# Kernel tuning notes

Measured on AMD Instinct MI355X. Metric: run time of the kernel, lower is better.

## Reference

```python
import jax, jax.numpy as jnp
import numpy as np

B, S = 64, 4096
IN_CH, HID, OUT_CH, LIFT, MODES, NLAYERS = 2, 64, 3, 256, 16, 4
FREQ = S // 2 + 1


def setup_inputs() -> dict:
    key = jax.random.key(0)
    ks = jax.random.split(key, 10)
    g = lambda k, shp, s=0.02: (jax.random.normal(k, shp, jnp.float32) * s)
    return {
        "x": jax.random.normal(ks[0], (B, S, IN_CH), jnp.float32),
        "lift_w1": g(ks[1], (LIFT, IN_CH), 0.1),
        "lift_b1": jnp.zeros((LIFT,), jnp.float32),
        "lift_w2": g(ks[2], (HID, LIFT)),
        "lift_b2": jnp.zeros((HID,), jnp.float32),
        # spectral weights per layer: real/imag parts of [in, out, modes]
        "spec_wr": g(ks[3], (NLAYERS, HID, HID, MODES), 1.0 / HID),
        "spec_wi": g(ks[4], (NLAYERS, HID, HID, MODES), 1.0 / HID),
        "skip_w": g(ks[5], (NLAYERS, HID, HID)),
        "skip_b": jnp.zeros((NLAYERS, HID), jnp.float32),
        "proj_w1": g(ks[6], (LIFT, HID)),
        "proj_b1": jnp.zeros((LIFT,), jnp.float32),
        "proj_w2": g(ks[7], (OUT_CH, LIFT)),
        "proj_b2": jnp.zeros((OUT_CH,), jnp.float32),
    }


def _gelu(x):
    return jax.nn.gelu(x, approximate=False)  # torch F.gelu default (exact)


def reference(x, lift_w1, lift_b1, lift_w2, lift_b2, spec_wr, spec_wi,
              skip_w, skip_b, proj_w1, proj_b1, proj_w2, proj_b2):
    # x: (B, S, 2) -> permute to channels-first (B, 2, S), fused into einsum
    h = jnp.einsum('bsi,oi->bos', x, lift_w1) + lift_b1[None, :, None]  # (B, 256, S)
    h = _gelu(h)
    h = jnp.einsum('bcs,oc->bos', h, lift_w2) + lift_b2[None, :, None]  # (B, 64, S)

    for l in range(NLAYERS):
        # spectral conv: rfft -> keep low modes -> complex mix -> irfft
        xf = jnp.fft.rfft(h, axis=-1)[..., :MODES]            # (B, HID, MODES) complex
        w = spec_wr[l] + 1j * spec_wi[l]                       # (HID, HID, MODES)
        yk = jnp.einsum('bim,iom->bom', xf, w)                 # (B, HID, MODES)
        yf = jnp.zeros((h.shape[0], HID, FREQ), jnp.complex64).at[..., :MODES].set(yk)
        spec = jnp.fft.irfft(yf, n=S, axis=-1)                 # (B, HID, S)
        skip = jnp.einsum('bcs,oc->bos', h, skip_w[l]) + skip_b[l][None, :, None]
        h = spec + skip
        if l < NLAYERS - 1:
            h = _gelu(h)

    h = _gelu(jnp.einsum('bcs,oc->bos', h, proj_w1) + proj_b1[None, :, None])
    out_seq = jnp.einsum('bcs,oc->bos', h, proj_w2) + proj_b2[None, :, None]  # (B, 3, S)
    # AdaptiveAvgPool1d(1) + squeeze(-1) == mean over length
    return out_seq.mean(axis=-1)  # (B, 3)
```

## Files before the change

### kernel.cpp

```cpp
#include <hip/hip_runtime.h>
#include <math.h>

#define B_    64
#define S_    4096
#define HID   64
#define LIFT  256
#define MODES 16
#define NL    4

#define OFF_H     0
#define OFF_ETB   16777216
#define OFF_XFY   (OFF_ETB + 131072)
#define OFF_SKH   (OFF_XFY + 131072)
#define OFF_SKL   (OFF_SKH + 8192)
#define OFF_W2HI  (OFF_SKL + 8192)
#define OFF_W2LO  (OFF_W2HI + 8192)
#define OFF_P1HI  (OFF_W2LO + 8192)
#define OFF_P1LO  (OFF_P1HI + 8192)
#define OFF_PART  (OFF_P1LO + 8192)
#define OFF_W1B   (OFF_PART + 12288)

typedef short short8 __attribute__((ext_vector_type(8)));
typedef float f32x4  __attribute__((ext_vector_type(4)));
typedef unsigned uint8v __attribute__((ext_vector_type(8)));
#define MFMA16 __builtin_amdgcn_mfma_f32_16x16x32_bf16

__device__ __forceinline__ float gelu_f(float x) {
  float z = fabsf(x) * 0.70710678118654752440f;
  float p = 1.0f + z * (0.0705230784f + z * (0.0422820123f +
            z * (0.0092705272f + z * (0.0001520143f +
            z * (0.0002765672f + z * 0.0000430638f)))));
  float r = __builtin_amdgcn_rcpf(p);
  r = r * r;
  r = r * r;
  r = r * r;
  r = r * r;
  float q = 0.5f * r;
  float phi = (x >= 0.0f) ? (1.0f - q) : q;
  return x * phi;
}
__device__ __forceinline__ unsigned short f2bf(float x) {
  unsigned u = __float_as_uint(x);
  u += 0x7fffu + ((u >> 16) & 1u);
  return (unsigned short)(u >> 16);
}
__device__ __forceinline__ float bf2f(unsigned short b) {
  return __uint_as_float(((unsigned)b) << 16);
}
__device__ __forceinline__ unsigned packsplit(float x) {
  unsigned short hi = f2bf(x);
  unsigned short lo = f2bf(x - bf2f(hi));
  return (unsigned)hi | ((unsigned)lo << 16);
}

__device__ __forceinline__ unsigned cvtpk2(float a, float b) {
  unsigned d;
  asm("v_cvt_pk_bf16_f32 %0, %1, %2" : "=v"(d) : "v"(a), "v"(b));
  return d;
}
__device__ __forceinline__ void split2pk(float a, float b,
                                         unsigned& hpk, unsigned& lpk) {
  hpk = cvtpk2(a, b);
  float ha = __uint_as_float(hpk << 16);
  float hb = __uint_as_float(hpk & 0xffff0000u);
  lpk = cvtpk2(a - ha, b - hb);
}
__device__ __forceinline__ void packsplit2(float a, float b,
                                           unsigned& ua, unsigned& ub) {
  unsigned hpk, lpk;
  split2pk(a, b, hpk, lpk);
  ua = __builtin_amdgcn_perm(lpk, hpk, 0x05040100u);
  ub = __builtin_amdgcn_perm(lpk, hpk, 0x07060302u);
}
__device__ __forceinline__ void unpk8(const unsigned* pk, short8& h8, short8& l8) {
  unsigned* hp = (unsigned*)&h8;
  unsigned* lp = (unsigned*)&l8;
  #pragma unroll
  for (int p = 0; p < 4; ++p) {
    hp[p] = __builtin_amdgcn_perm(pk[2*p+1], pk[2*p], 0x05040100u);
    lp[p] = __builtin_amdgcn_perm(pk[2*p+1], pk[2*p], 0x07060302u);
  }
}
__device__ __forceinline__ void unpk8v(const uint8v v, short8& h8, short8& l8) {
  unsigned* hp = (unsigned*)&h8;
  unsigned* lp = (unsigned*)&l8;
  #pragma unroll
  for (int p = 0; p < 4; ++p) {
    hp[p] = __builtin_amdgcn_perm(v[2*p+1], v[2*p], 0x05040100u);
    lp[p] = __builtin_amdgcn_perm(v[2*p+1], v[2*p], 0x07060302u);
  }
}

__global__ void k_init(const float* __restrict__ lift_w2,
                       const float* __restrict__ skip_w,
                       const float* __restrict__ proj_w1,
                       const float* __restrict__ lift_w1,
                       const float* __restrict__ lift_b1,
                       float* __restrict__ ws) {
  unsigned* etab = (unsigned*)(ws + OFF_ETB);
  unsigned short* skh = (unsigned short*)(ws + OFF_SKH);
  unsigned short* skl = (unsigned short*)(ws + OFF_SKL);
  unsigned short* w2hi = (unsigned short*)(ws + OFF_W2HI);
  unsigned short* w2lo = (unsigned short*)(ws + OFF_W2LO);
  unsigned short* p1hi = (unsigned short*)(ws + OFF_P1HI);
  unsigned short* p1lo = (unsigned short*)(ws + OFF_P1LO);
  float4* w1b = (float4*)(ws + OFF_W1B);
  int idx = blockIdx.x * 256 + threadIdx.x;
  int stride = gridDim.x * 256;
  for (int k = idx; k < 4096 * 32; k += stride) {
    int s = k >> 5, c = k & 31;
    int m = c & 15;
    int r = (m * s) & 4095;
    float th = (float)(2.0 * 3.14159265358979323846 / 4096.0) * (float)r;
    float sn, cn; sincosf(th, &sn, &cn);
    float v = (c < 16) ? cn : -sn;
    etab[k] = packsplit(v);
  }
  for (int k = idx; k < NL * HID * HID; k += stride) {
    float w = skip_w[k];
    unsigned short hi = f2bf(w);
    skh[k] = hi; skl[k] = f2bf(w - bf2f(hi));
  }
  for (int k = idx; k < HID * LIFT; k += stride) {
    float w = lift_w2[k];
    unsigned short hi = f2bf(w);
    w2hi[k] = hi; w2lo[k] = f2bf(w - bf2f(hi));
  }
  for (int k = idx; k < LIFT * HID; k += stride) {
    float w = proj_w1[k];
    unsigned short hi = f2bf(w);
    p1hi[k] = hi; p1lo[k] = f2bf(w - bf2f(hi));
  }
  for (int k = idx; k < LIFT; k += stride) {
    w1b[k] = make_float4(lift_w1[2 * k], lift_w1[2 * k + 1], lift_b1[k], 0.f);
  }
  for (int k = idx; k < 12288; k += stride)
    ws[OFF_PART + k] = 0.f;
}

__global__ __launch_bounds__(256, 2) void k_lift(
    const float* __restrict__ x, const float4* __restrict__ W1B,
    const float* __restrict__ b2,
    const unsigned short* __restrict__ Whi,
    const unsigned short* __restrict__ Wlo,
    unsigned* __restrict__ Hp) {
  int tid = threadIdx.x;
  int b = blockIdx.y, s0 = blockIdx.x * 256;
  int lane = tid & 63, wv = tid >> 6, quad = lane >> 4, n16 = lane & 15;
  int sw = s0 + wv * 64;
  int cq = quad * 8;
  float2 xv[4];
  #pragma unroll
  for (int nt = 0; nt < 4; ++nt)
    xv[nt] = ((const float2*)x)[b * S_ + sw + nt * 16 + n16];
  f32x4 acc[4][4];
  #pragma unroll
  for (int mt = 0; mt < 4; ++mt)
    #pragma unroll
    for (int nt = 0; nt < 4; ++nt) acc[mt][nt] = (f32x4){0.f, 0.f, 0.f, 0.f};

  #pragma unroll 1
  for (int k = 0; k < 8; ++k) {
    short8 ah[4], al[4];
    #pragma unroll
    for (int mt = 0; mt < 4; ++mt) {
      int aoff = (mt * 16 + n16) * 256 + k * 32 + cq;
      ah[mt] = *(const short8*)(Whi + aoff);
      al[mt] = *(const short8*)(Wlo + aoff);
    }
    float4 w[8];
    #pragma unroll
    for (int j = 0; j < 8; ++j) w[j] = W1B[k * 32 + cq + j];
    #pragma unroll
    for (int nt = 0; nt < 4; ++nt) {
      float t[8];
      #pragma unroll
      for (int j = 0; j < 8; ++j)
        t[j] = gelu_f(w[j].x * xv[nt].x + w[j].y * xv[nt].y + w[j].z);
      short8 bh, bl;
      unsigned* bhw = (unsigned*)&bh;
      unsigned* blw = (unsigned*)&bl;
      #pragma unroll
      for (int p = 0; p < 4; ++p)
        split2pk(t[2*p], t[2*p+1], bhw[p], blw[p]);
      #pragma unroll
      for (int mt = 0; mt < 4; ++mt) {
        acc[mt][nt] = MFMA16(ah[mt], bh, acc[mt][nt], 0, 0, 0);
        acc[mt][nt] = MFMA16(ah[mt], bl, acc[mt][nt], 0, 0, 0);
        acc[mt][nt] = MFMA16(al[mt], bh, acc[mt][nt], 0, 0, 0);
      }
    }
  }
  #pragma unroll
  for (int mt = 0; mt < 4; ++mt) {
    int o0 = mt * 16 + quad * 4;
    float4 bb = *(const float4*)&b2[o0];
    #pragma unroll
    for (int nt = 0; nt < 4; ++nt) {
      int sc = sw + nt * 16 + n16;
      unsigned* hp = Hp + ((size_t)b * HID + o0) * S_ + sc;
      unsigned u0, u1, u2, u3;
      packsplit2(acc[mt][nt][0] + bb.x, acc[mt][nt][1] + bb.y, u0, u1);
      packsplit2(acc[mt][nt][2] + bb.z, acc[mt][nt][3] + bb.w, u2, u3);
      hp[0]            = u0;
      hp[(size_t)S_]   = u1;
      hp[(size_t)2*S_] = u2;
      hp[(size_t)3*S_] = u3;
    }
  }
}

__global__ __launch_bounds__(256, 4) void k_fft_fwd(
    const unsigned* __restrict__ Hp, const unsigned* __restrict__ Etab,
    float* __restrict__ xf) {
  __shared__ float red[4 * 512];
  int tid = threadIdx.x;
  int i0 = blockIdx.x * 16, b = blockIdx.y, ks = blockIdx.z;
  int lane = tid & 63, wv = tid >> 6, quad = lane >> 4, n16 = lane & 15;
  const unsigned* hb = Hp + ((size_t)b * HID + i0 + n16) * S_;
  int g = ks * 4 + wv;
  f32x4 acc0 = (f32x4){0.f,0.f,0.f,0.f}, acc1 = (f32x4){0.f,0.f,0.f,0.f};
  #pragma unroll 1
  for (int kt = 0; kt < 8; ++kt) {
    int sb = g * 256 + kt * 32 + quad * 8;
    uint8v av = *(const uint8v*)(hb + sb);
    short8 ah, al;
    unpk8v(av, ah, al);
    unsigned q0[8], q1[8];
    #pragma unroll
    for (int j = 0; j < 8; ++j) {
      q0[j] = Etab[(sb + j) * 32 + n16];
      q1[j] = Etab[(sb + j) * 32 + 16 + n16];
    }
    short8 bh0, bl0, bh1, bl1;
    unpk8(q0, bh0, bl0);
    unpk8(q1, bh1, bl1);
    acc0 = MFMA16(ah, bh0, acc0, 0, 0, 0);
    acc0 = MFMA16(ah, bl0, acc0, 0, 0, 0);
    acc0 = MFMA16(al, bh0, acc0, 0, 0, 0);
    acc1 = MFMA16(ah, bh1, acc1, 0, 0, 0);
    acc1 = MFMA16(ah, bl1, acc1, 0, 0, 0);
    acc1 = MFMA16(al, bh1, acc1, 0, 0, 0);
  }
  #pragma unroll
  for (int r = 0; r < 4; ++r) {
    red[wv * 512 + (quad * 4 + r) * 32 + n16]      = acc0[r];
    red[wv * 512 + (quad * 4 + r) * 32 + 16 + n16] = acc1[r];
  }
  __syncthreads();
  #pragma unroll
  for (int u = 0; u < 2; ++u) {
    int t = u * 256 + tid;
    int il = t >> 5, c = t & 31;
    float v = red[t] + red[512 + t] + red[1024 + t] + red[1536 + t];
    atomicAdd(&xf[(size_t)b * 2048 + (i0 + il) * 32 + c], v);
  }
}

__global__ __launch_bounds__(256) void k_mix(
    const float* __restrict__ wr_, const float* __restrict__ wi_,
    float* __restrict__ xfy) {
  int tid = threadIdx.x;
  int b = blockIdx.x;
  __shared__ float xr[HID * MODES], xi[HID * MODES];
  const float* xfb = xfy + (size_t)b * 2048;
  for (int u = tid; u < HID * MODES; u += 256) {
    int i = u >> 4, m = u & 15;
    xr[u] = xfb[i * 32 + m];
    xi[u] = xfb[i * 32 + 16 + m];
  }
  __syncthreads();
  const float invS = 1.0f / (float)S_;
  unsigned* yk = (unsigned*)xfy + (size_t)b * 2048;
  #pragma unroll
  for (int pp = 0; pp < 4; ++pp) {
    int p = pp * 256 + tid;
    int o = p >> 4, m = p & 15;
    float yr = 0.f, yi = 0.f;
    for (int i2 = 0; i2 < HID; ++i2) {
      float wr = wr_[(i2 * HID + o) * MODES + m];
      float wi = wi_[(i2 * HID + o) * MODES + m];
      float xrv = xr[i2 * MODES + m], xiv = xi[i2 * MODES + m];
      yr += xrv * wr - xiv * wi;
      yi += xrv * wi + xiv * wr;
    }
    float fac = (m == 0) ? invS : 2.f * invS;
    unsigned ur, ui;
    packsplit2(yr * fac, yi * fac, ur, ui);
    yk[o * 32 + m]      = ur;
    yk[o * 32 + 16 + m] = ui;
  }
}

template <bool ACT>
__global__ __launch_bounds__(256, 2) void k_spec_skip(
    const unsigned short* __restrict__ Shi,
    const unsigned short* __restrict__ Slo,
    const float* __restrict__ skb,
    const unsigned* __restrict__ Yk,
    const unsigned* __restrict__ Etab,
    unsigned* __restrict__ Hp) {
  int tid = threadIdx.x;
  int s0 = blockIdx.x * 256, b = blockIdx.y;
  int lane = tid & 63, wv = tid >> 6, quad = lane >> 4, n16 = lane & 15;
  int sw = s0 + wv * 64;
  f32x4 acc[4][4];
  #pragma unroll
  for (int mt = 0; mt < 4; ++mt)
    #pragma unroll
    for (int nt = 0; nt < 4; ++nt) acc[mt][nt] = (f32x4){0.f,0.f,0.f,0.f};
  {
    short8 yh[4], yl[4];
    #pragma unroll
    for (int mt = 0; mt < 4; ++mt) {
      uint8v yv = *(const uint8v*)(Yk + (size_t)b * 2048 + (mt * 16 + n16) * 32 + quad * 8);
      unpk8v(yv, yh[mt], yl[mt]);
    }
    #pragma unroll
    for (int nt = 0; nt < 4; ++nt) {
      int sc = sw + nt * 16 + n16;
      uint8v tv = *(const uint8v*)(Etab + (size_t)sc * 32 + quad * 8);
      short8 th, tl;
      unpk8v(tv, th, tl);
      #pragma unroll
      for (int mt = 0; mt < 4; ++mt) {
        acc[mt][nt] = MFMA16(yh[mt], th, acc[mt][nt], 0, 0, 0);
        acc[mt][nt] = MFMA16(yh[mt], tl, acc[mt][nt], 0, 0, 0);
        acc[mt][nt] = MFMA16(yl[mt], th, acc[mt][nt], 0, 0, 0);
      }
    }
  }
  const unsigned* hb = Hp + (size_t)b * HID * S_;
  #pragma unroll
  for (int kk = 0; kk < 2; ++kk) {
    short8 skh[4], skl[4];
    #pragma unroll
    for (int mt = 0; mt < 4; ++mt) {
      int off = (mt * 16 + n16) * 64 + kk * 32 + quad * 8;
      skh[mt] = *(const short8*)(Shi + off);
      skl[mt] = *(const short8*)(Slo + off);
    }
    #pragma unroll
    for (int nt = 0; nt < 4; ++nt) {
      int sc = sw + nt * 16 + n16;
      unsigned pk[8];
      #pragma unroll
      for (int j = 0; j < 8; ++j)
        pk[j] = hb[(size_t)(kk * 32 + quad * 8 + j) * S_ + sc];
      short8 bh, bl;
      unpk8(pk, bh, bl);
      #pragma unroll
      for (int mt = 0; mt < 4; ++mt) {
        acc[mt][nt] = MFMA16(skh[mt], bh, acc[mt][nt], 0, 0, 0);
        acc[mt][nt] = MFMA16(skh[mt], bl, acc[mt][nt], 0, 0, 0);
        acc[mt][nt] = MFMA16(skl[mt], bh, acc[mt][nt], 0, 0, 0);
      }
    }
  }
  #pragma unroll
  for (int mt = 0; mt < 4; ++mt) {
    int o0 = mt * 16 + quad * 4;
    float4 bb = *(const float4*)&skb[o0];
    #pragma unroll
    for (int nt = 0; nt < 4; ++nt) {
      int sc = sw + nt * 16 + n16;
      float v0 = acc[mt][nt][0] + bb.x;
      float v1 = acc[mt][nt][1] + bb.y;
      float v2 = acc[mt][nt][2] + bb.z;
      float v3 = acc[mt][nt][3] + bb.w;
      if (ACT) { v0 = gelu_f(v0); v1 = gelu_f(v1); v2 = gelu_f(v2); v3 = gelu_f(v3); }
      unsigned u0, u1, u2, u3;
      packsplit2(v0, v1, u0, u1);
      packsplit2(v2, v3, u2, u3);
      unsigned* hp = Hp + ((size_t)b * HID + o0) * S_ + sc;
      hp[0]            = u0;
      hp[(size_t)S_]   = u1;
      hp[(size_t)2*S_] = u2;
      hp[(size_t)3*S_] = u3;
    }
  }
}

__global__ __launch_bounds__(256, 2) void k_proj(
    const unsigned short* __restrict__ Phi,
    const unsigned short* __restrict__ Plo,
    const float* __restrict__ pb1, const float* __restrict__ pw2,
    const unsigned* __restrict__ Hp, float* __restrict__ part) {
  __shared__ unsigned Bp[64 * 65];
  __shared__ float red[12];
  int tid = threadIdx.x;
  int s0 = blockIdx.x * 64, b = blockIdx.y;
  int lane = tid & 63, wv = tid >> 6, quad = lane >> 4, n16 = lane & 15;
  #pragma unroll
  for (int u = 0; u < 16; ++u) {
    int idx = u * 256 + tid;
    int c = idx >> 6, s = idx & 63;
    Bp[c * 65 + s] = Hp[((size_t)b * HID + c) * S_ + s0 + s];
  }
  __syncthreads();
  int m0 = blockIdx.z * 128 + wv * 32;
  f32x4 acc[2][4];
  #pragma unroll
  for (int mt = 0; mt < 2; ++mt)
    #pragma unroll
    for (int nt = 0; nt < 4; ++nt) acc[mt][nt] = (f32x4){0.f,0.f,0.f,0.f};
  #pragma unroll
  for (int kk = 0; kk < 2; ++kk) {
    int kbase = kk * 32 + quad * 8;
    short8 ah[2], al[2];
    #pragma unroll
    for (int mt = 0; mt < 2; ++mt) {
      int aoff = (m0 + mt * 16 + n16) * 64 + kbase;
      ah[mt] = *(const short8*)(Phi + aoff);
      al[mt] = *(const short8*)(Plo + aoff);
    }
    #pragma unroll
    for (int nt = 0; nt < 4; ++nt) {
      int sc = nt * 16 + n16;
      unsigned pk[8];
      #pragma unroll
      for (int j = 0; j < 8; ++j) pk[j] = Bp[(kbase + j) * 65 + sc];
      short8 bh, bl;
      unpk8(pk, bh, bl);
      #pragma unroll
      for (int mt = 0; mt < 2; ++mt) {
        acc[mt][nt] = MFMA16(ah[mt], bh, acc[mt][nt], 0, 0, 0);
        acc[mt][nt] = MFMA16(ah[mt], bl, acc[mt][nt], 0, 0, 0);
        acc[mt][nt] = MFMA16(al[mt], bh, acc[mt][nt], 0, 0, 0);
      }
    }
  }
  float o0 = 0.f, o1 = 0.f, o2 = 0.f;
  #pragma unroll
  for (int mt = 0; mt < 2; ++mt) {
    int c2b = m0 + mt * 16 + quad * 4;
    float4 bb = *(const float4*)&pb1[c2b];
    float4 p0 = *(const float4*)&pw2[c2b];
    float4 p1 = *(const float4*)&pw2[256 + c2b];
    float4 p2 = *(const float4*)&pw2[512 + c2b];
    #pragma unroll
    for (int nt = 0; nt < 4; ++nt) {
      f32x4 a = acc[mt][nt];
      float t0 = gelu_f(a[0] + bb.x);
      float t1 = gelu_f(a[1] + bb.y);
      float t2 = gelu_f(a[2] + bb.z);
      float t3 = gelu_f(a[3] + bb.w);
      o0 += p0.x * t0 + p0.y * t1 + p0.z * t2 + p0.w * t3;
      o1 += p1.x * t0 + p1.y * t1 + p1.z * t2 + p1.w * t3;
      o2 += p2.x * t0 + p2.y * t1 + p2.z * t2 + p2.w * t3;
    }
  }
  #pragma unroll
  for (int off = 32; off > 0; off >>= 1) {
    o0 += __shfl_xor(o0, off, 64);
    o1 += __shfl_xor(o1, off, 64);
    o2 += __shfl_xor(o2, off, 64);
  }
  if (lane == 0) { red[wv*3+0] = o0; red[wv*3+1] = o1; red[wv*3+2] = o2; }
  __syncthreads();
  if (tid < 3) {
    float sum = red[tid] + red[3 + tid] + red[6 + tid] + red[9 + tid];
    atomicAdd(&part[(b * 64 + blockIdx.x) * 3 + tid], sum);
  }
}

__global__ void k_final(const float* __restrict__ part,
                        const float* __restrict__ pb2,
                        float* __restrict__ out) {
  int t = threadIdx.x;
  if (t < B_ * 3) {
    int b = t / 3, j = t % 3;
    float s = 0.f;
    for (int k = 0; k < 64; ++k) s += part[(b * 64 + k) * 3 + j];
    out[t] = s * (1.0f / (float)S_) + pb2[j];
  }
}

extern "C" void kernel_launch(void* const* d_in, const int* in_sizes, int n_in,
                              void* d_out, int out_size, void* d_ws, size_t ws_size,
                              hipStream_t stream) {
  const float* x   = (const float*)d_in[0];
  const float* lw1 = (const float*)d_in[1];
  const float* lb1 = (const float*)d_in[2];
  const float* lw2 = (const float*)d_in[3];
  const float* lb2 = (const float*)d_in[4];
  const float* swr = (const float*)d_in[5];
  const float* swi = (const float*)d_in[6];
  const float* skw = (const float*)d_in[7];
  const float* skb = (const float*)d_in[8];
  const float* pw1 = (const float*)d_in[9];
  const float* pb1 = (const float*)d_in[10];
  const float* pw2 = (const float*)d_in[11];
  const float* pb2 = (const float*)d_in[12];
  float* ws = (float*)d_ws;
  unsigned* Hp  = (unsigned*)(ws + OFF_H);
  unsigned* ETB = (unsigned*)(ws + OFF_ETB);
  float*    XFY = ws + OFF_XFY;

  k_init<<<256, 256, 0, stream>>>(lw2, skw, pw1, lw1, lb1, ws);
  k_lift<<<dim3(S_ / 256, B_), 256, 0, stream>>>(
      x, (const float4*)(ws + OFF_W1B), lb2,
      (const unsigned short*)(ws + OFF_W2HI),
      (const unsigned short*)(ws + OFF_W2LO), Hp);
  for (int l = 0; l < NL; ++l) {
    hipMemsetAsync(XFY, 0, (size_t)B_ * 2048 * sizeof(float), stream);
    k_fft_fwd<<<dim3(4, B_, 4), 256, 0, stream>>>(Hp, ETB, XFY);
    k_mix<<<B_, 256, 0, stream>>>(swr + l * HID * HID * MODES,
                                  swi + l * HID * HID * MODES, XFY);
    if (l < NL - 1)
      k_spec_skip<true><<<dim3(S_ / 256, B_), 256, 0, stream>>>(
          (const unsigned short*)(ws + OFF_SKH) + l * HID * HID,
          (const unsigned short*)(ws + OFF_SKL) + l * HID * HID,
          skb + l * HID, (const unsigned*)XFY, ETB, Hp);
    else
      k_spec_skip<false><<<dim3(S_ / 256, B_), 256, 0, stream>>>(
          (const unsigned short*)(ws + OFF_SKH) + l * HID * HID,
          (const unsigned short*)(ws + OFF_SKL) + l * HID * HID,
          skb + l * HID, (const unsigned*)XFY, ETB, Hp);
  }
  k_proj<<<dim3(S_ / 64, B_, 2), 256, 0, stream>>>(
      (const unsigned short*)(ws + OFF_P1HI),
      (const unsigned short*)(ws + OFF_P1LO),
      pb1, pw2, Hp, ws + OFF_PART);
  k_final<<<1, 256, 0, stream>>>(ws + OFF_PART, pb2, (float*)d_out);
}
```

Before: 516.2 us.

## Reorder projection: sum GELU activations per channel before applying proj_w2

```diff
diff --git a/kernel.cpp b/kernel.cpp
--- a/kernel.cpp
+++ b/kernel.cpp
@@ -18,7 +18,7 @@
 #define OFF_P1HI  (OFF_W2LO + 8192)
 #define OFF_P1LO  (OFF_P1HI + 8192)
 #define OFF_PART  (OFF_P1LO + 8192)
-#define OFF_W1B   (OFF_PART + 12288)
+#define OFF_W1B   (OFF_PART + 16384)
 
 typedef short short8 __attribute__((ext_vector_type(8)));
 typedef float f32x4  __attribute__((ext_vector_type(4)));
@@ -134,7 +134,7 @@
   for (int k = idx; k < LIFT; k += stride) {
     w1b[k] = make_float4(lift_w1[2 * k], lift_w1[2 * k + 1], lift_b1[k], 0.f);
   }
-  for (int k = idx; k < 12288; k += stride)
+  for (int k = idx; k < 16384; k += stride)
     ws[OFF_PART + k] = 0.f;
 }
 
@@ -384,18 +384,22 @@
 __global__ __launch_bounds__(256, 2) void k_proj(
     const unsigned short* __restrict__ Phi,
     const unsigned short* __restrict__ Plo,
-    const float* __restrict__ pb1, const float* __restrict__ pw2,
-    const unsigned* __restrict__ Hp, float* __restrict__ part) {
-  __shared__ unsigned Bp[64 * 65];
-  __shared__ float red[12];
+    const float* __restrict__ pb1,
+    const unsigned* __restrict__ Hp, float* __restrict__ gsum) {
+  __shared__ unsigned BpH[64 * 34];
+  __shared__ unsigned BpL[64 * 34];
   int tid = threadIdx.x;
   int s0 = blockIdx.x * 64, b = blockIdx.y;
   int lane = tid & 63, wv = tid >> 6, quad = lane >> 4, n16 = lane & 15;
-  #pragma unroll
-  for (int u = 0; u < 16; ++u) {
-    int idx = u * 256 + tid;
-    int c = idx >> 6, s = idx & 63;
-    Bp[c * 65 + s] = Hp[((size_t)b * HID + c) * S_ + s0 + s];
+  {
+    const unsigned* hpb = Hp + ((size_t)b * HID + wv * 16) * S_ + s0 + lane;
+    #pragma unroll
+    for (int up = 0; up < 8; ++up) {
+      unsigned u0 = hpb[(size_t)(2 * up) * S_];
+      unsigned u1 = hpb[(size_t)(2 * up + 1) * S_];
+      BpH[lane * 34 + wv * 8 + up] = __builtin_amdgcn_perm(u1, u0, 0x05040100u);
+      BpL[lane * 34 + wv * 8 + up] = __builtin_amdgcn_perm(u1, u0, 0x07060302u);
+    }
   }
   __syncthreads();
   int m0 = blockIdx.z * 128 + wv * 32;
@@ -406,50 +410,75 @@
     for (int nt = 0; nt < 4; ++nt) acc[mt][nt] = (f32x4){0.f,0.f,0.f,0.f};
   #pragma unroll
   for (int kk = 0; kk < 2; ++kk) {
-    int kbase = kk * 32 + quad * 8;
+    int kb = kk * 16 + quad * 4;
     short8 ah[2], al[2];
     #pragma unroll
     for (int mt = 0; mt < 2; ++mt) {
-      int aoff = (m0 + mt * 16 + n16) * 64 + kbase;
+      int aoff = (m0 + mt * 16 + n16) * 64 + kk * 32 + quad * 8;
       ah[mt] = *(const short8*)(Phi + aoff);
       al[mt] = *(const short8*)(Plo + aoff);
     }
     #pragma unroll
     for (int nt = 0; nt < 4; ++nt) {
       int sc = nt * 16 + n16;
-      unsigned pk[8];
-      #pragma unroll
-      for (int j = 0; j < 8; ++j) pk[j] = Bp[(kbase + j) * 65 + sc];
-      short8 bh, bl;
-      unpk8(pk, bh, bl);
+      union { unsigned u[4]; short8 s; } Bh, Bl;
+      *(uint2*)&Bh.u[0] = *(const uint2*)&BpH[sc * 34 + kb];
+      *(uint2*)&Bh.u[2] = *(const uint2*)&BpH[sc * 34 + kb + 2];
+      *(uint2*)&Bl.u[0] = *(const uint2*)&BpL[sc * 34 + kb];
+      *(uint2*)&Bl.u[2] = *(const uint2*)&BpL[sc * 34 + kb + 2];
       #pragma unroll
       for (int mt = 0; mt < 2; ++mt) {
-        acc[mt][nt] = MFMA16(ah[mt], bh, acc[mt][nt], 0, 0, 0);
-        acc[mt][nt] = MFMA16(ah[mt], bl, acc[mt][nt], 0, 0, 0);
-        acc[mt][nt] = MFMA16(al[mt], bh, acc[mt][nt], 0, 0, 0);
+        acc[mt][nt] = MFMA16(ah[mt], Bh.s, acc[mt][nt], 0, 0, 0);
+        acc[mt][nt] = MFMA16(ah[mt], Bl.s, acc[mt][nt], 0, 0, 0);
+        acc[mt][nt] = MFMA16(al[mt], Bh.s, acc[mt][nt], 0, 0, 0);
       }
     }
   }
-  float o0 = 0.f, o1 = 0.f, o2 = 0.f;
+  float rs[2][4];
   #pragma unroll
   for (int mt = 0; mt < 2; ++mt) {
     int c2b = m0 + mt * 16 + quad * 4;
     float4 bb = *(const float4*)&pb1[c2b];
-    float4 p0 = *(const float4*)&pw2[c2b];
-    float4 p1 = *(const float4*)&pw2[256 + c2b];
-    float4 p2 = *(const float4*)&pw2[512 + c2b];
+    rs[mt][0] = rs[mt][1] = rs[mt][2] = rs[mt][3] = 0.f;
     #pragma unroll
     for (int nt = 0; nt < 4; ++nt) {
       f32x4 a = acc[mt][nt];
-      float t0 = gelu_f(a[0] + bb.x);
-      float t1 = gelu_f(a[1] + bb.y);
-      float t2 = gelu_f(a[2] + bb.z);
-      float t3 = gelu_f(a[3] + bb.w);
-      o0 += p0.x * t0 + p0.y * t1 + p0.z * t2 + p0.w * t3;
-      o1 += p1.x * t0 + p1.y * t1 + p1.z * t2 + p1.w * t3;
-      o2 += p2.x * t0 + p2.y * t1 + p2.z * t2 + p2.w * t3;
-    }
-  }
+      rs[mt][0] += gelu_f(a[0] + bb.x);
+      rs[mt][1] += gelu_f(a[1] + bb.y);
+      rs[mt][2] += gelu_f(a[2] + bb.z);
+      rs[mt][3] += gelu_f(a[3] + bb.w);
+    }
+  }
+  #pragma unroll
+  for (int off = 1; off < 16; off <<= 1) {
+    #pragma unroll
+    for (int mt = 0; mt < 2; ++mt)
+      #pragma unroll
+      for (int r = 0; r < 4; ++r)
+        rs[mt][r] += __shfl_xor(rs[mt][r], off, 16);
+  }
+  if (n16 == 0) {
+    #pragma unroll
+    for (int mt = 0; mt < 2; ++mt) {
+      int c2b = m0 + mt * 16 + quad * 4;
+      #pragma unroll
+      for (int r = 0; r < 4; ++r)
+        atomicAdd(&gsum[b * 256 + c2b + r], rs[mt][r]);
+    }
+  }
+}
+
+__global__ void k_final(const float* __restrict__ gsum,
+                        const float* __restrict__ pw2,
+                        const float* __restrict__ pb2,
+                        float* __restrict__ out) {
+  __shared__ float red[12];
+  int tid = threadIdx.x, b = blockIdx.x;
+  int lane = tid & 63, wv = tid >> 6;
+  float g = gsum[b * 256 + tid];
+  float o0 = pw2[tid] * g;
+  float o1 = pw2[256 + tid] * g;
+  float o2 = pw2[512 + tid] * g;
   #pragma unroll
   for (int off = 32; off > 0; off >>= 1) {
     o0 += __shfl_xor(o0, off, 64);
@@ -459,20 +488,8 @@
   if (lane == 0) { red[wv*3+0] = o0; red[wv*3+1] = o1; red[wv*3+2] = o2; }
   __syncthreads();
   if (tid < 3) {
-    float sum = red[tid] + red[3 + tid] + red[6 + tid] + red[9 + tid];
-    atomicAdd(&part[(b * 64 + blockIdx.x) * 3 + tid], sum);
-  }
-}
-
-__global__ void k_final(const float* __restrict__ part,
-                        const float* __restrict__ pb2,
-                        float* __restrict__ out) {
-  int t = threadIdx.x;
-  if (t < B_ * 3) {
-    int b = t / 3, j = t % 3;
-    float s = 0.f;
-    for (int k = 0; k < 64; ++k) s += part[(b * 64 + k) * 3 + j];
-    out[t] = s * (1.0f / (float)S_) + pb2[j];
+    float s = red[tid] + red[3 + tid] + red[6 + tid] + red[9 + tid];
+    out[b * 3 + tid] = s * (1.0f / (float)S_) + pb2[tid];
   }
 }
 
@@ -521,6 +538,6 @@
   k_proj<<<dim3(S_ / 64, B_, 2), 256, 0, stream>>>(
       (const unsigned short*)(ws + OFF_P1HI),
       (const unsigned short*)(ws + OFF_P1LO),
-      pb1, pw2, Hp, ws + OFF_PART);
-  k_final<<<1, 256, 0, stream>>>(ws + OFF_PART, pb2, (float*)d_out);
-}
+      pb1, Hp, ws + OFF_PART);
+  k_final<<<B_, 256, 0, stream>>>(ws + OFF_PART, pw2, pb2, (float*)d_out);
+}
```

New measurement: 522.0 us. Within noise of the previous version (+1.1%).
